# Kernel tuning notes

Measured on AMD Instinct MI355X. Metric: run time of the kernel, lower is better.

## Reference

```python
import jax, jax.numpy as jnp
import numpy as np

B, L, D = 4096, 50, 64
NU, NI, NR = 100000, 100000, 5


def setup_inputs() -> dict:
    key = jax.random.key(0)
    ks = jax.random.split(key, 16)
    s = 0.02
    inp = {
        "nodes_v": jax.random.randint(ks[0], (B,), 0, NI),
        "neigh_u": jax.random.randint(ks[1], (B, L), 0, NU),
        "neigh_r": jax.random.randint(ks[2], (B, L), 0, NR),
        "embed_u": jax.random.normal(ks[3], (NU, D)) * s,
        "embed_i": jax.random.normal(ks[4], (NI, D)) * s,
        "embed_r": jax.random.normal(ks[5], (NR, D)) * s,
        # gv MLP: Linear(2D,D) ReLU Linear(D,D) ReLU Linear(D,D)
        "gv_w1": jax.random.normal(ks[6], (2 * D, D)) * s, "gv_b1": jnp.zeros((D,)),
        "gv_w2": jax.random.normal(ks[7], (D, D)) * s,     "gv_b2": jnp.zeros((D,)),
        "gv_w3": jax.random.normal(ks[8], (D, D)) * s,     "gv_b3": jnp.zeros((D,)),
        # attention MLP: Linear(2D,D) ReLU Linear(D,D) ReLU Linear(D,1), softmax over neighbors
        "att_w1": jax.random.normal(ks[9], (2 * D, D)) * s, "att_b1": jnp.zeros((D,)),
        "att_w2": jax.random.normal(ks[10], (D, D)) * s,    "att_b2": jnp.zeros((D,)),
        "att_w3": jax.random.normal(ks[11], (D, 1)) * s,    "att_b3": jnp.zeros((1,)),
        # combine: Linear(2D,D) ReLU Linear(D,D) ReLU
        "wr1_w": jax.random.normal(ks[12], (2 * D, D)) * s, "wr1_b": jnp.zeros((D,)),
        "wr2_w": jax.random.normal(ks[13], (D, D)) * s,     "wr2_b": jnp.zeros((D,)),
    }
    return inp


def reference(nodes_v, neigh_u, neigh_r, embed_u, embed_i, embed_r,
              gv_w1, gv_b1, gv_w2, gv_b2, gv_w3, gv_b3,
              att_w1, att_b1, att_w2, att_b2, att_w3, att_b3,
              wr1_w, wr1_b, wr2_w, wr2_b):
    qj = embed_i[nodes_v]            # [B, D] item reps
    pt = embed_u[neigh_u]            # [B, L, D] neighbor user reps
    er = embed_r[neigh_r]            # [B, L, D] rating reps
    # fusion MLP g(.)
    x = jnp.concatenate([pt, er], axis=-1)                    # [B, L, 2D]
    h = jax.nn.relu(x @ gv_w1 + gv_b1)
    h = jax.nn.relu(h @ gv_w2 + gv_b2)
    fjt = h @ gv_w3 + gv_b3                                   # [B, L, D]
    # attention over neighbors (dropout is identity in eval mode)
    q_rep = jnp.broadcast_to(qj[:, None, :], fjt.shape)       # [B, L, D]
    a = jnp.concatenate([fjt, q_rep], axis=-1)                # [B, L, 2D]
    a = jax.nn.relu(a @ att_w1 + att_b1)
    a = jax.nn.relu(a @ att_w2 + att_b2)
    scores = (a @ att_w3 + att_b3)[..., 0]                    # [B, L]
    mu = jax.nn.softmax(scores, axis=1)                       # softmax over neighbors
    zj = jnp.einsum("bld,bl->bd", fjt, mu)                   # weighted aggregation
    # combine aggregated neighborhood with item's own embedding (2D -> D)
    z = jax.nn.relu(jnp.concatenate([zj, qj], axis=-1) @ wr1_w + wr1_b)
    out = jax.nn.relu(z @ wr2_w + wr2_b)                      # [B, D]
    return out
```

## Files before the change

### kernel.cpp

```cpp
#include <hip/hip_runtime.h>

typedef __bf16 bf16;
typedef short s16x8 __attribute__((ext_vector_type(8)));
typedef __bf16 b16x8 __attribute__((ext_vector_type(8)));
typedef float f32x4 __attribute__((ext_vector_type(4)));

#define B_   4096
#define L_   50
#define LP   64
#define SX   136

#define OFF_W1F  0
#define OFF_W2F  8192
#define OFF_W3F  12288
#define OFF_WCF  16384
#define OFF_A2F  20480
#define OFF_R1T  24576
#define OFF_R2T  32768
#define WT_TOTAL 36864
#define BIAS1P_BYTE 73728
#define CQ_BYTE     73984

#define PREP_W_BLOCKS 145
#define PREP_C_BLOCKS 1024

__device__ __forceinline__ unsigned short f2b(float f) {
    __bf16 h = (__bf16)f;
    return __builtin_bit_cast(unsigned short, h);
}
__device__ __forceinline__ unsigned pack2(float a, float b) {
    return (unsigned)f2b(a) | ((unsigned)f2b(b) << 16);
}

template<int KT, bool RELU>
__device__ __forceinline__ void dual_layer(const bf16* A0, const bf16* A1,
                                           const bf16* __restrict__ Wf,
                                           const float* __restrict__ bias,
                                           bf16* O0, bf16* O1, int lane)
{
    const int m = lane & 15, quad = lane >> 4;
    f32x4 ac0[4] = {}, ac1[4] = {};
#pragma unroll
    for (int kt = 0; kt < KT; ++kt) {
        s16x8 a0 = *(const s16x8*)(A0 + m * SX + kt * 32 + quad * 8);
        s16x8 a1 = *(const s16x8*)(A1 + m * SX + kt * 32 + quad * 8);
#pragma unroll
        for (int nt = 0; nt < 4; ++nt) {
            s16x8 b = *(const s16x8*)(Wf + (kt * 4 + nt) * 512 + lane * 8);
            ac0[nt] = __builtin_amdgcn_mfma_f32_16x16x32_bf16(a0, b, ac0[nt], 0, 0, 0);
            ac1[nt] = __builtin_amdgcn_mfma_f32_16x16x32_bf16(a1, b, ac1[nt], 0, 0, 0);
        }
    }
#pragma unroll
    for (int nt = 0; nt < 4; ++nt) {
        int c = nt * 16 + m;
        float bv = bias[c];
#pragma unroll
        for (int r4 = 0; r4 < 4; ++r4) {
            float v0 = ac0[nt][r4] + bv, v1 = ac1[nt][r4] + bv;
            if (RELU) { v0 = fmaxf(v0, 0.f); v1 = fmaxf(v1, 0.f); }
            O0[(quad * 4 + r4) * SX + c] = (bf16)v0;
            O1[(quad * 4 + r4) * SX + c] = (bf16)v1;
        }
    }
}

extern "C" __global__ void prep_all(const float* __restrict__ w1, const float* __restrict__ w2,
                                    const float* __restrict__ w3, const float* __restrict__ a1,
                                    const float* __restrict__ a2, const float* __restrict__ r1,
                                    const float* __restrict__ r2, const float* __restrict__ gb3,
                                    const float* __restrict__ ab1,
                                    const int* __restrict__ nodes_v, const float* __restrict__ embed_i,
                                    bf16* __restrict__ wt, float* __restrict__ bias1p,
                                    float* __restrict__ cq)
{
    if (blockIdx.x >= PREP_W_BLOCKS) {
        int gid = (blockIdx.x - PREP_W_BLOCKS) * 256 + threadIdx.x;
        int b = gid >> 6, n = gid & 63;
        int v = nodes_v[b];
        const float* q = embed_i + v * 64;
        float s0 = 0.f, s1 = 0.f, s2 = 0.f, s3 = 0.f;
#pragma unroll
        for (int k = 0; k < 64; k += 4) {
            s0 = fmaf(q[k],     a1[(64 + k) * 64 + n],     s0);
            s1 = fmaf(q[k + 1], a1[(64 + k + 1) * 64 + n], s1);
            s2 = fmaf(q[k + 2], a1[(64 + k + 2) * 64 + n], s2);
            s3 = fmaf(q[k + 3], a1[(64 + k + 3) * 64 + n], s3);
        }
        cq[gid] = (s0 + s1) + (s2 + s3);
        return;
    }
    int i = blockIdx.x * 256 + threadIdx.x;
    if (i >= WT_TOTAL + 64) return;
    if (i >= WT_TOTAL) {
        int n = i - WT_TOTAL;
        float s0 = ab1[n], s1 = 0.f, s2 = 0.f, s3 = 0.f;
#pragma unroll
        for (int t = 0; t < 64; t += 4) {
            s0 = fmaf(gb3[t],     a1[t * 64 + n],       s0);
            s1 = fmaf(gb3[t + 1], a1[(t + 1) * 64 + n], s1);
            s2 = fmaf(gb3[t + 2], a1[(t + 2) * 64 + n], s2);
            s3 = fmaf(gb3[t + 3], a1[(t + 3) * 64 + n], s3);
        }
        bias1p[n] = (s0 + s1) + (s2 + s3);
        return;
    }
    float val;
    if (i < OFF_R1T) {
        int off, kind;
        if      (i < OFF_W2F) { off = OFF_W1F; kind = 0; }
        else if (i < OFF_W3F) { off = OFF_W2F; kind = 1; }
        else if (i < OFF_WCF) { off = OFF_W3F; kind = 2; }
        else if (i < OFF_A2F) { off = OFF_WCF; kind = 3; }
        else                  { off = OFF_A2F; kind = 4; }
        int local = i - off;
        int f = local >> 9, lane = (local >> 3) & 63, j = local & 7;
        int kt = f >> 2, nt = f & 3, quad = lane >> 4, m = lane & 15;
        int k = kt * 32 + quad * 8 + j;
        int n = nt * 16 + m;
        if (kind == 0)      val = w1[k * 64 + n];
        else if (kind == 1) val = w2[k * 64 + n];
        else if (kind == 2) val = w3[k * 64 + n];
        else if (kind == 4) val = a2[k * 64 + n];
        else {
            float s0 = 0.f, s1 = 0.f, s2 = 0.f, s3 = 0.f;
#pragma unroll
            for (int t = 0; t < 64; t += 4) {
                float4 w = *(const float4*)(w3 + k * 64 + t);
                s0 = fmaf(w.x, a1[t * 64 + n],       s0);
                s1 = fmaf(w.y, a1[(t + 1) * 64 + n], s1);
                s2 = fmaf(w.z, a1[(t + 2) * 64 + n], s2);
                s3 = fmaf(w.w, a1[(t + 3) * 64 + n], s3);
            }
            val = (s0 + s1) + (s2 + s3);
        }
    }
    else if (i < OFF_R2T) { int li = i - OFF_R1T; int n = li >> 7, k = li & 127; val = r1[k * 64 + n]; }
    else                  { int li = i - OFF_R2T; int n = li >> 6, k = li & 63;  val = r2[k * 64 + n]; }
    wt[i] = (bf16)val;
}

extern "C" __global__ void __launch_bounds__(256, 2)
dense_fused(const int* __restrict__ nodes_v, const int* __restrict__ neigh_u,
            const int* __restrict__ neigh_r,
            const float* __restrict__ embed_u, const float* __restrict__ embed_i,
            const float* __restrict__ embed_r,
            const float* __restrict__ gv_b1, const float* __restrict__ gv_b2,
            const float* __restrict__ gv_b3,
            const float* __restrict__ att_b2, const float* __restrict__ att_w3,
            const float* __restrict__ wr1_b, const float* __restrict__ wr2_b,
            const bf16* __restrict__ wt, const float* __restrict__ cq,
            const float* __restrict__ bias1p, float* __restrict__ out)
{
    __shared__ __align__(16) bf16 Xs[128 * SX];
    __shared__ float csS[128];
    __shared__ float qsh[128];
    __shared__ float scs[128];
    __shared__ float zp[4 * 64];

    const int tid = threadIdx.x;
    const int lane = tid & 63, wave = tid >> 6;
    const int m = lane & 15, quad = lane >> 4;
    const int b0 = blockIdx.x * 2;
    const int rw0 = wave * 32;

    if (tid < 128) {
        int item = tid >> 6, n = tid & 63;
        csS[tid] = cq[(b0 + item) * 64 + n] + bias1p[n];
        qsh[tid] = embed_i[nodes_v[b0 + item] * 64 + n];
    }

    {
        const int rsub = lane >> 4;
        const int c = lane & 15;
#pragma unroll
        for (int it = 0; it < 8; ++it) {
            int rloc = rw0 + it * 4 + rsub;
            int item = rloc >> 6, l = rloc & 63;
            float4 vu = make_float4(0.f, 0.f, 0.f, 0.f), vr = vu;
            if (l < L_) {
                int u = neigh_u[(b0 + item) * L_ + l];
                int r = neigh_r[(b0 + item) * L_ + l];
                vu = *(const float4*)(embed_u + u * 64 + c * 4);
                vr = *(const float4*)(embed_r + r * 64 + c * 4);
            }
            uint2 pu, pr;
            pu.x = pack2(vu.x, vu.y); pu.y = pack2(vu.z, vu.w);
            pr.x = pack2(vr.x, vr.y); pr.y = pack2(vr.z, vr.w);
            *(uint2*)(Xs + rloc * SX + c * 4) = pu;
            *(uint2*)(Xs + rloc * SX + 64 + c * 4) = pr;
        }
    }

    bf16* X0 = Xs + rw0 * SX;
    bf16* X1 = Xs + (rw0 + 16) * SX;

    dual_layer<4, true>(X0, X1, wt + OFF_W1F, gv_b1, X0 + 64, X1 + 64, lane);

    __syncthreads();

    dual_layer<2, true>(X0 + 64, X1 + 64, wt + OFF_W2F, gv_b2, X0, X1, lane);

    {
        const bf16* w3f = wt + OFF_W3F;
        const bf16* wcf = wt + OFF_WCF;
        const int io = (rw0 >> 6) * 64;
        f32x4 aF0[4] = {}, aF1[4] = {}, aA0[4] = {}, aA1[4] = {};
#pragma unroll
        for (int kt = 0; kt < 2; ++kt) {
            s16x8 a0 = *(const s16x8*)(X0 + m * SX + kt * 32 + quad * 8);
            s16x8 a1 = *(const s16x8*)(X1 + m * SX + kt * 32 + quad * 8);
#pragma unroll
            for (int nt = 0; nt < 4; ++nt) {
                s16x8 bF = *(const s16x8*)(w3f + (kt * 4 + nt) * 512 + lane * 8);
                s16x8 bA = *(const s16x8*)(wcf + (kt * 4 + nt) * 512 + lane * 8);
                aF0[nt] = __builtin_amdgcn_mfma_f32_16x16x32_bf16(a0, bF, aF0[nt], 0, 0, 0);
                aF1[nt] = __builtin_amdgcn_mfma_f32_16x16x32_bf16(a1, bF, aF1[nt], 0, 0, 0);
                aA0[nt] = __builtin_amdgcn_mfma_f32_16x16x32_bf16(a0, bA, aA0[nt], 0, 0, 0);
                aA1[nt] = __builtin_amdgcn_mfma_f32_16x16x32_bf16(a1, bA, aA1[nt], 0, 0, 0);
            }
        }
#pragma unroll
        for (int nt = 0; nt < 4; ++nt) {
            int c = nt * 16 + m;
            float b3v = gv_b3[c], b1v = csS[io + c];
#pragma unroll
            for (int r4 = 0; r4 < 4; ++r4) {
                int rl0 = rw0 + quad * 4 + r4, rl1 = rl0 + 16;
                Xs[rl0 * SX + 64 + c] = (bf16)(aF0[nt][r4] + b3v);
                Xs[rl1 * SX + 64 + c] = (bf16)(aF1[nt][r4] + b3v);
                Xs[rl0 * SX + c] = (bf16)fmaxf(aA0[nt][r4] + b1v, 0.f);
                Xs[rl1 * SX + c] = (bf16)fmaxf(aA1[nt][r4] + b1v, 0.f);
            }
        }
    }

    {
        const bf16* a2f = wt + OFF_A2F;
        f32x4 ac0[4] = {}, ac1[4] = {};
#pragma unroll
        for (int kt = 0; kt < 2; ++kt) {
            s16x8 a0 = *(const s16x8*)(X0 + m * SX + kt * 32 + quad * 8);
            s16x8 a1 = *(const s16x8*)(X1 + m * SX + kt * 32 + quad * 8);
#pragma unroll
            for (int nt = 0; nt < 4; ++nt) {
                s16x8 b = *(const s16x8*)(a2f + (kt * 4 + nt) * 512 + lane * 8);
                ac0[nt] = __builtin_amdgcn_mfma_f32_16x16x32_bf16(a0, b, ac0[nt], 0, 0, 0);
                ac1[nt] = __builtin_amdgcn_mfma_f32_16x16x32_bf16(a1, b, ac1[nt], 0, 0, 0);
            }
        }
        float s0[4] = {0.f, 0.f, 0.f, 0.f}, s1[4] = {0.f, 0.f, 0.f, 0.f};
#pragma unroll
        for (int nt = 0; nt < 4; ++nt) {
            int c = nt * 16 + m;
            float b2v = att_b2[c], w3v = att_w3[c];
#pragma unroll
            for (int r4 = 0; r4 < 4; ++r4) {
                s0[r4] += fmaxf(ac0[nt][r4] + b2v, 0.f) * w3v;
                s1[r4] += fmaxf(ac1[nt][r4] + b2v, 0.f) * w3v;
            }
        }
#pragma unroll
        for (int mask = 1; mask < 16; mask <<= 1)
#pragma unroll
            for (int r4 = 0; r4 < 4; ++r4) {
                s0[r4] += __shfl_xor(s0[r4], mask);
                s1[r4] += __shfl_xor(s1[r4], mask);
            }
        if (m == 0) {
#pragma unroll
            for (int r4 = 0; r4 < 4; ++r4) {
                scs[rw0 + quad * 4 + r4] = s0[r4];
                scs[rw0 + 16 + quad * 4 + r4] = s1[r4];
            }
        }
    }
    __syncthreads();

    {
        const int io = (rw0 >> 6) * 64;
        float s = (lane < L_) ? scs[io + lane] : -1e30f;
        float mx = s;
#pragma unroll
        for (int off = 32; off; off >>= 1) mx = fmaxf(mx, __shfl_xor(mx, off));
        float e = (lane < L_) ? __expf(s - mx) : 0.f;
        float sum = e;
#pragma unroll
        for (int off = 32; off; off >>= 1) sum += __shfl_xor(sum, off);
        float mu = e / sum;

        float z = 0.f;
#pragma unroll
        for (int i = 0; i < 32; ++i) {
            int rloc = rw0 + i;
            z += (float)Xs[rloc * SX + 64 + lane] * __shfl(mu, (rloc & 63));
        }
        zp[wave * 64 + lane] = z;
    }
    __syncthreads();

    if ((wave & 1) == 0) {
        const int item = wave >> 1;
        const int d = lane;
        float z = zp[(wave + 0) * 64 + d] + zp[(wave + 1) * 64 + d];
        float* zsh = scs + item * 64;
        zsh[d] = z;

        float accz = wr1_b[d];
        const bf16* r1 = wt + OFF_R1T + d * 128;
#pragma unroll
        for (int k8 = 0; k8 < 8; ++k8) {
            b16x8 wv = *(const b16x8*)(r1 + k8 * 8);
#pragma unroll
            for (int j = 0; j < 8; ++j) accz = fmaf((float)wv[j], zsh[k8 * 8 + j], accz);
        }
#pragma unroll
        for (int k8 = 0; k8 < 8; ++k8) {
            b16x8 wv = *(const b16x8*)(r1 + 64 + k8 * 8);
#pragma unroll
            for (int j = 0; j < 8; ++j) accz = fmaf((float)wv[j], qsh[item * 64 + k8 * 8 + j], accz);
        }
        float* z2sh = zp + wave * 64;
        z2sh[d] = fmaxf(accz, 0.f);

        float acco = wr2_b[d];
        const bf16* r2 = wt + OFF_R2T + d * 64;
#pragma unroll
        for (int k8 = 0; k8 < 8; ++k8) {
            b16x8 wv = *(const b16x8*)(r2 + k8 * 8);
#pragma unroll
            for (int j = 0; j < 8; ++j) acco = fmaf((float)wv[j], z2sh[k8 * 8 + j], acco);
        }
        out[(b0 + item) * 64 + d] = fmaxf(acco, 0.f);
    }
}

extern "C" void kernel_launch(void* const* d_in, const int* in_sizes, int n_in,
                              void* d_out, int out_size, void* d_ws, size_t ws_size,
                              hipStream_t stream)
{
    const int* nodes_v = (const int*)d_in[0];
    const int* neigh_u = (const int*)d_in[1];
    const int* neigh_r = (const int*)d_in[2];
    const float* embed_u = (const float*)d_in[3];
    const float* embed_i = (const float*)d_in[4];
    const float* embed_r = (const float*)d_in[5];
    const float* gv_w1  = (const float*)d_in[6];  const float* gv_b1 = (const float*)d_in[7];
    const float* gv_w2  = (const float*)d_in[8];  const float* gv_b2 = (const float*)d_in[9];
    const float* gv_w3  = (const float*)d_in[10]; const float* gv_b3 = (const float*)d_in[11];
    const float* att_w1 = (const float*)d_in[12]; const float* att_b1 = (const float*)d_in[13];
    const float* att_w2 = (const float*)d_in[14]; const float* att_b2 = (const float*)d_in[15];
    const float* att_w3 = (const float*)d_in[16]; const float* att_b3 = (const float*)d_in[17];
    const float* wr1_w  = (const float*)d_in[18]; const float* wr1_b = (const float*)d_in[19];
    const float* wr2_w  = (const float*)d_in[20]; const float* wr2_b = (const float*)d_in[21];
    (void)att_b3;

    bf16*  wt     = (bf16*)d_ws;
    float* bias1p = (float*)((char*)d_ws + BIAS1P_BYTE);
    float* cq     = (float*)((char*)d_ws + CQ_BYTE);

    prep_all<<<PREP_W_BLOCKS + PREP_C_BLOCKS, 256, 0, stream>>>(
        gv_w1, gv_w2, gv_w3, att_w1, att_w2, wr1_w, wr2_w, gv_b3, att_b1,
        nodes_v, embed_i, wt, bias1p, cq);
    dense_fused<<<B_ / 2, 256, 0, stream>>>(nodes_v, neigh_u, neigh_r,
                                            embed_u, embed_i, embed_r,
                                            gv_b1, gv_b2, gv_b3, att_b2, att_w3,
                                            wr1_b, wr2_b, wt, cq, bias1p, (float*)d_out);
}
```

Measured before the change: 169.7 us.

## Feed first layer from global gathers directly and keep fjt in registers

The first MLP layer now builds its MFMA A-fragments straight from the gathered fp32 embedding rows, so the 128x136 LDS staging buffer shrinks to a 72-wide hidden buffer. The fjt output (layer 3) stays in accumulator registers and the softmax-weighted aggregation runs on them with shuffles, with the gv_b3 bias folded in afterwards since the softmax weights sum to one. This is meant to cut LDS traffic and footprint, which may raise occupancy. In exchange, padded rows now read clamped duplicate neighbours, and each lane issues strided uncoalesced float4 loads directly into the MFMA path.

New measurement: 169.3 us. Within noise of the previous version (-0.2%).

```diff
diff --git a/kernel.cpp b/kernel.cpp
--- a/kernel.cpp
+++ b/kernel.cpp
@@ -7,8 +7,7 @@
 
 #define B_   4096
 #define L_   50
-#define LP   64
-#define SX   136
+#define SH   72
 
 #define OFF_W1F  0
 #define OFF_W2F  8192
@@ -31,24 +30,33 @@
 __device__ __forceinline__ unsigned pack2(float a, float b) {
     return (unsigned)f2b(a) | ((unsigned)f2b(b) << 16);
 }
-
-template<int KT, bool RELU>
-__device__ __forceinline__ void dual_layer(const bf16* A0, const bf16* A1,
-                                           const bf16* __restrict__ Wf,
-                                           const float* __restrict__ bias,
-                                           bf16* O0, bf16* O1, int lane)
+__device__ __forceinline__ s16x8 mkfrag(float4 a, float4 b) {
+    union { s16x8 v; unsigned u[4]; } r;
+    r.u[0] = pack2(a.x, a.y); r.u[1] = pack2(a.z, a.w);
+    r.u[2] = pack2(b.x, b.y); r.u[3] = pack2(b.z, b.w);
+    return r.v;
+}
+__device__ __forceinline__ f32x4 mfma16(s16x8 a, s16x8 b, f32x4 c) {
+    return __builtin_amdgcn_mfma_f32_16x16x32_bf16(a, b, c, 0, 0, 0);
+}
+
+template<bool RELU>
+__device__ __forceinline__ void dual_layer_lds(const bf16* A0, const bf16* A1,
+                                               const bf16* __restrict__ Wf,
+                                               const float* __restrict__ bias,
+                                               bf16* O0, bf16* O1, int lane)
 {
     const int m = lane & 15, quad = lane >> 4;
     f32x4 ac0[4] = {}, ac1[4] = {};
 #pragma unroll
-    for (int kt = 0; kt < KT; ++kt) {
-        s16x8 a0 = *(const s16x8*)(A0 + m * SX + kt * 32 + quad * 8);
-        s16x8 a1 = *(const s16x8*)(A1 + m * SX + kt * 32 + quad * 8);
+    for (int kt = 0; kt < 2; ++kt) {
+        s16x8 a0 = *(const s16x8*)(A0 + m * SH + kt * 32 + quad * 8);
+        s16x8 a1 = *(const s16x8*)(A1 + m * SH + kt * 32 + quad * 8);
 #pragma unroll
         for (int nt = 0; nt < 4; ++nt) {
             s16x8 b = *(const s16x8*)(Wf + (kt * 4 + nt) * 512 + lane * 8);
-            ac0[nt] = __builtin_amdgcn_mfma_f32_16x16x32_bf16(a0, b, ac0[nt], 0, 0, 0);
-            ac1[nt] = __builtin_amdgcn_mfma_f32_16x16x32_bf16(a1, b, ac1[nt], 0, 0, 0);
+            ac0[nt] = mfma16(a0, b, ac0[nt]);
+            ac1[nt] = mfma16(a1, b, ac1[nt]);
         }
     }
 #pragma unroll
@@ -59,8 +67,8 @@
         for (int r4 = 0; r4 < 4; ++r4) {
             float v0 = ac0[nt][r4] + bv, v1 = ac1[nt][r4] + bv;
             if (RELU) { v0 = fmaxf(v0, 0.f); v1 = fmaxf(v1, 0.f); }
-            O0[(quad * 4 + r4) * SX + c] = (bf16)v0;
-            O1[(quad * 4 + r4) * SX + c] = (bf16)v1;
+            O0[(quad * 4 + r4) * SH + c] = (bf16)v0;
+            O1[(quad * 4 + r4) * SH + c] = (bf16)v1;
         }
     }
 }
@@ -152,7 +160,7 @@
             const bf16* __restrict__ wt, const float* __restrict__ cq,
             const float* __restrict__ bias1p, float* __restrict__ out)
 {
-    __shared__ __align__(16) bf16 Xs[128 * SX];
+    __shared__ __align__(16) bf16 H[128 * SH];
     __shared__ float csS[128];
     __shared__ float qsh[128];
     __shared__ float scs[128];
@@ -163,6 +171,8 @@
     const int m = lane & 15, quad = lane >> 4;
     const int b0 = blockIdx.x * 2;
     const int rw0 = wave * 32;
+    const int item_w = rw0 >> 6;
+    const int lbase = rw0 & 63;
 
     if (tid < 128) {
         int item = tid >> 6, n = tid & 63;
@@ -170,67 +180,80 @@
         qsh[tid] = embed_i[nodes_v[b0 + item] * 64 + n];
     }
 
+    const int bw = b0 + item_w;
+    const int l0 = min(lbase + m, L_ - 1);
+    const int l1 = min(lbase + 16 + m, L_ - 1);
+    const int u0 = neigh_u[bw * L_ + l0], u1 = neigh_u[bw * L_ + l1];
+    const int v0 = neigh_r[bw * L_ + l0], v1 = neigh_r[bw * L_ + l1];
+
+    bf16* Hw = H + rw0 * SH;
+    bf16* H0 = Hw;
+    bf16* H1 = Hw + 16 * SH;
+
     {
-        const int rsub = lane >> 4;
-        const int c = lane & 15;
-#pragma unroll
-        for (int it = 0; it < 8; ++it) {
-            int rloc = rw0 + it * 4 + rsub;
-            int item = rloc >> 6, l = rloc & 63;
-            float4 vu = make_float4(0.f, 0.f, 0.f, 0.f), vr = vu;
-            if (l < L_) {
-                int u = neigh_u[(b0 + item) * L_ + l];
-                int r = neigh_r[(b0 + item) * L_ + l];
-                vu = *(const float4*)(embed_u + u * 64 + c * 4);
-                vr = *(const float4*)(embed_r + r * 64 + c * 4);
-            }
-            uint2 pu, pr;
-            pu.x = pack2(vu.x, vu.y); pu.y = pack2(vu.z, vu.w);
-            pr.x = pack2(vr.x, vr.y); pr.y = pack2(vr.z, vr.w);
-            *(uint2*)(Xs + rloc * SX + c * 4) = pu;
-            *(uint2*)(Xs + rloc * SX + 64 + c * 4) = pr;
-        }
-    }
-
-    bf16* X0 = Xs + rw0 * SX;
-    bf16* X1 = Xs + (rw0 + 16) * SX;
-
-    dual_layer<4, true>(X0, X1, wt + OFF_W1F, gv_b1, X0 + 64, X1 + 64, lane);
+        const float* b00 = embed_u + u0 * 64;
+        const float* b01 = embed_u + u1 * 64;
+        const float* b10 = embed_r + v0 * 64;
+        const float* b11 = embed_r + v1 * 64;
+        f32x4 ac0[4] = {}, ac1[4] = {};
+#pragma unroll
+        for (int kt = 0; kt < 4; ++kt) {
+            const float* s0p = (kt < 2 ? b00 : b10) + (kt & 1) * 32 + quad * 8;
+            const float* s1p = (kt < 2 ? b01 : b11) + (kt & 1) * 32 + quad * 8;
+            float4 a0a = *(const float4*)s0p, a0b = *(const float4*)(s0p + 4);
+            float4 a1a = *(const float4*)s1p, a1b = *(const float4*)(s1p + 4);
+            s16x8 a0 = mkfrag(a0a, a0b);
+            s16x8 a1 = mkfrag(a1a, a1b);
+#pragma unroll
+            for (int nt = 0; nt < 4; ++nt) {
+                s16x8 b = *(const s16x8*)(wt + OFF_W1F + (kt * 4 + nt) * 512 + lane * 8);
+                ac0[nt] = mfma16(a0, b, ac0[nt]);
+                ac1[nt] = mfma16(a1, b, ac1[nt]);
+            }
+        }
+#pragma unroll
+        for (int nt = 0; nt < 4; ++nt) {
+            int c = nt * 16 + m;
+            float bv = gv_b1[c];
+#pragma unroll
+            for (int r4 = 0; r4 < 4; ++r4) {
+                H0[(quad * 4 + r4) * SH + c] = (bf16)fmaxf(ac0[nt][r4] + bv, 0.f);
+                H1[(quad * 4 + r4) * SH + c] = (bf16)fmaxf(ac1[nt][r4] + bv, 0.f);
+            }
+        }
+    }
+
+    dual_layer_lds<true>(H0, H1, wt + OFF_W2F, gv_b2, H0, H1, lane);
 
     __syncthreads();
 
-    dual_layer<2, true>(X0 + 64, X1 + 64, wt + OFF_W2F, gv_b2, X0, X1, lane);
-
+    f32x4 aF0[4] = {}, aF1[4] = {};
     {
         const bf16* w3f = wt + OFF_W3F;
         const bf16* wcf = wt + OFF_WCF;
-        const int io = (rw0 >> 6) * 64;
-        f32x4 aF0[4] = {}, aF1[4] = {}, aA0[4] = {}, aA1[4] = {};
+        f32x4 aA0[4] = {}, aA1[4] = {};
 #pragma unroll
         for (int kt = 0; kt < 2; ++kt) {
-            s16x8 a0 = *(const s16x8*)(X0 + m * SX + kt * 32 + quad * 8);
-            s16x8 a1 = *(const s16x8*)(X1 + m * SX + kt * 32 + quad * 8);
+            s16x8 a0 = *(const s16x8*)(H0 + m * SH + kt * 32 + quad * 8);
+            s16x8 a1 = *(const s16x8*)(H1 + m * SH + kt * 32 + quad * 8);
 #pragma unroll
             for (int nt = 0; nt < 4; ++nt) {
                 s16x8 bF = *(const s16x8*)(w3f + (kt * 4 + nt) * 512 + lane * 8);
                 s16x8 bA = *(const s16x8*)(wcf + (kt * 4 + nt) * 512 + lane * 8);
-                aF0[nt] = __builtin_amdgcn_mfma_f32_16x16x32_bf16(a0, bF, aF0[nt], 0, 0, 0);
-                aF1[nt] = __builtin_amdgcn_mfma_f32_16x16x32_bf16(a1, bF, aF1[nt], 0, 0, 0);
-                aA0[nt] = __builtin_amdgcn_mfma_f32_16x16x32_bf16(a0, bA, aA0[nt], 0, 0, 0);
-                aA1[nt] = __builtin_amdgcn_mfma_f32_16x16x32_bf16(a1, bA, aA1[nt], 0, 0, 0);
+                aF0[nt] = mfma16(a0, bF, aF0[nt]);
+                aF1[nt] = mfma16(a1, bF, aF1[nt]);
+                aA0[nt] = mfma16(a0, bA, aA0[nt]);
+                aA1[nt] = mfma16(a1, bA, aA1[nt]);
             }
         }
 #pragma unroll
         for (int nt = 0; nt < 4; ++nt) {
             int c = nt * 16 + m;
-            float b3v = gv_b3[c], b1v = csS[io + c];
+            float b1v = csS[item_w * 64 + c];
 #pragma unroll
             for (int r4 = 0; r4 < 4; ++r4) {
-                int rl0 = rw0 + quad * 4 + r4, rl1 = rl0 + 16;
-                Xs[rl0 * SX + 64 + c] = (bf16)(aF0[nt][r4] + b3v);
-                Xs[rl1 * SX + 64 + c] = (bf16)(aF1[nt][r4] + b3v);
-                Xs[rl0 * SX + c] = (bf16)fmaxf(aA0[nt][r4] + b1v, 0.f);
-                Xs[rl1 * SX + c] = (bf16)fmaxf(aA1[nt][r4] + b1v, 0.f);
+                H0[(quad * 4 + r4) * SH + c] = (bf16)fmaxf(aA0[nt][r4] + b1v, 0.f);
+                H1[(quad * 4 + r4) * SH + c] = (bf16)fmaxf(aA1[nt][r4] + b1v, 0.f);
             }
         }
     }
@@ -240,13 +263,13 @@
         f32x4 ac0[4] = {}, ac1[4] = {};
 #pragma unroll
         for (int kt = 0; kt < 2; ++kt) {
-            s16x8 a0 = *(const s16x8*)(X0 + m * SX + kt * 32 + quad * 8);
-            s16x8 a1 = *(const s16x8*)(X1 + m * SX + kt * 32 + quad * 8);
+            s16x8 a0 = *(const s16x8*)(H0 + m * SH + kt * 32 + quad * 8);
+            s16x8 a1 = *(const s16x8*)(H1 + m * SH + kt * 32 + quad * 8);
 #pragma unroll
             for (int nt = 0; nt < 4; ++nt) {
                 s16x8 b = *(const s16x8*)(a2f + (kt * 4 + nt) * 512 + lane * 8);
-                ac0[nt] = __builtin_amdgcn_mfma_f32_16x16x32_bf16(a0, b, ac0[nt], 0, 0, 0);
-                ac1[nt] = __builtin_amdgcn_mfma_f32_16x16x32_bf16(a1, b, ac1[nt], 0, 0, 0);
+                ac0[nt] = mfma16(a0, b, ac0[nt]);
+                ac1[nt] = mfma16(a1, b, ac1[nt]);
             }
         }
         float s0[4] = {0.f, 0.f, 0.f, 0.f}, s1[4] = {0.f, 0.f, 0.f, 0.f};
@@ -270,16 +293,15 @@
         if (m == 0) {
 #pragma unroll
             for (int r4 = 0; r4 < 4; ++r4) {
-                scs[rw0 + quad * 4 + r4] = s0[r4];
-                scs[rw0 + 16 + quad * 4 + r4] = s1[r4];
+                scs[item_w * 64 + lbase + quad * 4 + r4] = s0[r4];
+                scs[item_w * 64 + lbase + 16 + quad * 4 + r4] = s1[r4];
             }
         }
     }
     __syncthreads();
 
     {
-        const int io = (rw0 >> 6) * 64;
-        float s = (lane < L_) ? scs[io + lane] : -1e30f;
+        float s = (lane < L_) ? scs[item_w * 64 + lane] : -1e30f;
         float mx = s;
 #pragma unroll
         for (int off = 32; off; off >>= 1) mx = fmaxf(mx, __shfl_xor(mx, off));
@@ -289,20 +311,31 @@
         for (int off = 32; off; off >>= 1) sum += __shfl_xor(sum, off);
         float mu = e / sum;
 
-        float z = 0.f;
-#pragma unroll
-        for (int i = 0; i < 32; ++i) {
-            int rloc = rw0 + i;
-            z += (float)Xs[rloc * SX + 64 + lane] * __shfl(mu, (rloc & 63));
-        }
-        zp[wave * 64 + lane] = z;
+        float z[4] = {0.f, 0.f, 0.f, 0.f};
+#pragma unroll
+        for (int r4 = 0; r4 < 4; ++r4) {
+            float m0 = __shfl(mu, lbase + quad * 4 + r4);
+            float m1 = __shfl(mu, lbase + 16 + quad * 4 + r4);
+#pragma unroll
+            for (int nt = 0; nt < 4; ++nt)
+                z[nt] += aF0[nt][r4] * m0 + aF1[nt][r4] * m1;
+        }
+#pragma unroll
+        for (int nt = 0; nt < 4; ++nt) {
+            z[nt] += __shfl_xor(z[nt], 16);
+            z[nt] += __shfl_xor(z[nt], 32);
+        }
+        if (quad == 0) {
+#pragma unroll
+            for (int nt = 0; nt < 4; ++nt) zp[wave * 64 + nt * 16 + m] = z[nt];
+        }
     }
     __syncthreads();
 
     if ((wave & 1) == 0) {
         const int item = wave >> 1;
         const int d = lane;
-        float z = zp[(wave + 0) * 64 + d] + zp[(wave + 1) * 64 + d];
+        float z = zp[wave * 64 + d] + zp[wave * 64 + 64 + d] + gv_b3[d];
         float* zsh = scs + item * 64;
         zsh[d] = z;
 
```
